# Kernel optimization log

Hardware: AMD Instinct MI355X
Metric: run time of the kernel (lower is better)

The kernel has to match this reference:

```python
import jax, jax.numpy as jnp
import numpy as np

LUT_VALS = np.array([-1.0, -0.5, -0.333333, -0.2, -0.142857, -0.090909, -0.076923,
                     0.0, 0.076923, 0.090909, 0.142857, 0.2, 0.333333, 0.5, 1.0],
                    dtype=np.float32)

B, S, IN, OUT = 4, 2048, 2048, 8192


def setup_inputs() -> dict:
    key = jax.random.key(0)
    kx, ki = jax.random.split(key)
    x = jax.random.normal(kx, (B, S, IN), dtype=jnp.float32)
    # uint8 LUT indices into the 15-entry primal grid (stored int32 for jax indexing)
    grid_indices = jax.random.randint(ki, (OUT, IN), 0, 15, dtype=jnp.int32)
    scale = jnp.float32(1.0)
    lut = jnp.asarray(LUT_VALS)
    return {"x": x, "grid_indices": grid_indices, "scale": scale, "lut": lut}


def reference(x, grid_indices, scale, lut):
    # Dequantize: gather LUT values by index, then scalar scale (GhostQuantFunction.forward)
    weights = lut[grid_indices] * scale          # [OUT, IN] fp32
    # F.linear(x, weights): y = x @ W^T
    return jnp.einsum('bsi,oi->bso', x, weights)
```

## Files before the change

kernel.cpp:

```cpp
#include <hip/hip_runtime.h>
#include <cstdint>

typedef short bf16x8 __attribute__((ext_vector_type(8)));
typedef unsigned short u16x8 __attribute__((ext_vector_type(8)));
typedef float f32x4 __attribute__((ext_vector_type(4)));
typedef __attribute__((address_space(3))) uint32_t lds_u32;
typedef const __attribute__((address_space(1))) uint32_t gbl_u32;

__device__ __forceinline__ unsigned short f2bf(float f) {
  union { float f; uint32_t u; } c; c.f = f;
  uint32_t u = c.u;
  return (unsigned short)((u + 0x7fffu + ((u >> 16) & 1u)) >> 16);
}

__global__ void cvt_x_kernel(const float* __restrict__ x,
                             unsigned short* __restrict__ y, long n) {
  long t = (long)blockIdx.x * blockDim.x + threadIdx.x;
  long base = t * 8;
  if (base >= n) return;
  const float4* p = (const float4*)(x + base);
  float4 f0 = p[0], f1 = p[1];
  u16x8 v;
  v[0] = f2bf(f0.x); v[1] = f2bf(f0.y); v[2] = f2bf(f0.z); v[3] = f2bf(f0.w);
  v[4] = f2bf(f1.x); v[5] = f2bf(f1.y); v[6] = f2bf(f1.z); v[7] = f2bf(f1.w);
  *(u16x8*)(y + base) = v;
}

__global__ void dequant_kernel(const int* __restrict__ idx,
                               const float* __restrict__ lut,
                               const float* __restrict__ scale,
                               unsigned short* __restrict__ w, long n) {
  __shared__ unsigned short slut[16];
  if (threadIdx.x < 15) slut[threadIdx.x] = f2bf(lut[threadIdx.x] * scale[0]);
  __syncthreads();
  long t = (long)blockIdx.x * blockDim.x + threadIdx.x;
  long base = t * 8;
  if (base >= n) return;
  const int4* p = (const int4*)(idx + base);
  int4 i0 = p[0], i1 = p[1];
  u16x8 v;
  v[0] = slut[i0.x]; v[1] = slut[i0.y]; v[2] = slut[i0.z]; v[3] = slut[i0.w];
  v[4] = slut[i1.x]; v[5] = slut[i1.y]; v[6] = slut[i1.z]; v[7] = slut[i1.w];
  *(u16x8*)(w + base) = v;
}

__global__ __launch_bounds__(256) void gemm_bt(
    const unsigned short* __restrict__ A,
    const unsigned short* __restrict__ B,
    float* __restrict__ C, int M, int N, int K) {
  __shared__ unsigned short lA[128 * 32];
  __shared__ unsigned short lB[128 * 32];

  const int t = threadIdx.x;
  const int l = t & 63;
  const int w = t >> 6;
  const int wm = w >> 1, wn = w & 1;
  const int bm = blockIdx.y, bn = blockIdx.x;

  f32x4 acc[4][4] = {};

  const unsigned short* gA = A + (size_t)(bm * 128 + (t >> 2)) * K + (t & 3) * 8;
  const unsigned short* gB = B + (size_t)(bn * 128 + (t >> 2)) * K + (t & 3) * 8;
  lds_u32* sA = (lds_u32*)(&lA[0]) + t * 4;
  lds_u32* sB = (lds_u32*)(&lB[0]) + t * 4;

  const int ar = wm * 64 + (l & 15);
  const int br = wn * 64 + (l & 15);
  const int ak = (l >> 4) * 8;

  for (int kt = 0; kt < K; kt += 32) {
    __syncthreads();
    __builtin_amdgcn_global_load_lds((gbl_u32*)(gA + kt),          sA,        16, 0, 0);
    __builtin_amdgcn_global_load_lds((gbl_u32*)(gA + 64 * K + kt), sA + 1024, 16, 0, 0);
    __builtin_amdgcn_global_load_lds((gbl_u32*)(gB + kt),          sB,        16, 0, 0);
    __builtin_amdgcn_global_load_lds((gbl_u32*)(gB + 64 * K + kt), sB + 1024, 16, 0, 0);
    __syncthreads();

    bf16x8 af[4], bfr[4];
#pragma unroll
    for (int i = 0; i < 4; ++i)
      af[i] = *(const bf16x8*)&lA[(ar + i * 16) * 32 + ak];
#pragma unroll
    for (int j = 0; j < 4; ++j)
      bfr[j] = *(const bf16x8*)&lB[(br + j * 16) * 32 + ak];
#pragma unroll
    for (int i = 0; i < 4; ++i)
#pragma unroll
      for (int j = 0; j < 4; ++j)
        acc[i][j] = __builtin_amdgcn_mfma_f32_16x16x32_bf16(af[i], bfr[j], acc[i][j], 0, 0, 0);
  }

  float* Cp = C + (size_t)(bm * 128 + wm * 64 + (l >> 4) * 4) * N
              + bn * 128 + wn * 64 + (l & 15);
#pragma unroll
  for (int i = 0; i < 4; ++i)
#pragma unroll
    for (int j = 0; j < 4; ++j)
#pragma unroll
      for (int r = 0; r < 4; ++r)
        Cp[(size_t)(i * 16 + r) * N + j * 16] = acc[i][j][r];
}

extern "C" void kernel_launch(void* const* d_in, const int* in_sizes, int n_in,
                              void* d_out, int out_size, void* d_ws, size_t ws_size,
                              hipStream_t stream) {
  const float* x     = (const float*)d_in[0];
  const int*   gi    = (const int*)d_in[1];
  const float* scale = (const float*)d_in[2];
  const float* lut   = (const float*)d_in[3];
  float* out = (float*)d_out;

  const int M = 8192, N = 8192, K = 2048;
  unsigned short* xb = (unsigned short*)d_ws;
  unsigned short* wb = xb + (size_t)M * K;

  long nx = (long)M * K;
  long nw = (long)N * K;
  cvt_x_kernel<<<dim3((unsigned)(nx / (256 * 8))), dim3(256), 0, stream>>>(x, xb, nx);
  dequant_kernel<<<dim3((unsigned)(nw / (256 * 8))), dim3(256), 0, stream>>>(gi, lut, scale, wb, nw);

  dim3 grid(N / 128, M / 128);
  gemm_bt<<<grid, dim3(256), 0, stream>>>(xb, wb, out, M, N, K);
}
```

Baseline: 665.2 us.

## Fuse prep kernels, use shuffle LUT, and swizzle GEMM block order

```diff
diff --git a/kernel.cpp b/kernel.cpp
--- a/kernel.cpp
+++ b/kernel.cpp
@@ -13,35 +13,40 @@
   return (unsigned short)((u + 0x7fffu + ((u >> 16) & 1u)) >> 16);
 }
 
-__global__ void cvt_x_kernel(const float* __restrict__ x,
-                             unsigned short* __restrict__ y, long n) {
-  long t = (long)blockIdx.x * blockDim.x + threadIdx.x;
-  long base = t * 8;
-  if (base >= n) return;
-  const float4* p = (const float4*)(x + base);
-  float4 f0 = p[0], f1 = p[1];
-  u16x8 v;
-  v[0] = f2bf(f0.x); v[1] = f2bf(f0.y); v[2] = f2bf(f0.z); v[3] = f2bf(f0.w);
-  v[4] = f2bf(f1.x); v[5] = f2bf(f1.y); v[6] = f2bf(f1.z); v[7] = f2bf(f1.w);
-  *(u16x8*)(y + base) = v;
-}
-
-__global__ void dequant_kernel(const int* __restrict__ idx,
-                               const float* __restrict__ lut,
-                               const float* __restrict__ scale,
-                               unsigned short* __restrict__ w, long n) {
-  __shared__ unsigned short slut[16];
-  if (threadIdx.x < 15) slut[threadIdx.x] = f2bf(lut[threadIdx.x] * scale[0]);
-  __syncthreads();
-  long t = (long)blockIdx.x * blockDim.x + threadIdx.x;
-  long base = t * 8;
-  if (base >= n) return;
-  const int4* p = (const int4*)(idx + base);
-  int4 i0 = p[0], i1 = p[1];
-  u16x8 v;
-  v[0] = slut[i0.x]; v[1] = slut[i0.y]; v[2] = slut[i0.z]; v[3] = slut[i0.w];
-  v[4] = slut[i1.x]; v[5] = slut[i1.y]; v[6] = slut[i1.z]; v[7] = slut[i1.w];
-  *(u16x8*)(w + base) = v;
+__global__ void prep_kernel(const float* __restrict__ x,
+                            const int* __restrict__ gidx,
+                            const float* __restrict__ lut,
+                            const float* __restrict__ scale,
+                            unsigned short* __restrict__ xb,
+                            unsigned short* __restrict__ wb,
+                            long nx) {
+  long bid = blockIdx.x;
+  long xblocks = nx / 2048;
+  if (bid < xblocks) {
+    long base = (bid * 256 + threadIdx.x) * 8;
+    const float4* p = (const float4*)(x + base);
+    float4 f0 = p[0], f1 = p[1];
+    u16x8 v;
+    v[0] = f2bf(f0.x); v[1] = f2bf(f0.y); v[2] = f2bf(f0.z); v[3] = f2bf(f0.w);
+    v[4] = f2bf(f1.x); v[5] = f2bf(f1.y); v[6] = f2bf(f1.z); v[7] = f2bf(f1.w);
+    *(u16x8*)(xb + base) = v;
+  } else {
+    int li = threadIdx.x & 15; if (li > 14) li = 14;
+    int ubf = (int)f2bf(lut[li] * scale[0]);
+    long base = ((bid - xblocks) * 256 + threadIdx.x) * 8;
+    const int4* p = (const int4*)(gidx + base);
+    int4 i0 = p[0], i1 = p[1];
+    u16x8 v;
+    v[0] = (unsigned short)__shfl(ubf, i0.x);
+    v[1] = (unsigned short)__shfl(ubf, i0.y);
+    v[2] = (unsigned short)__shfl(ubf, i0.z);
+    v[3] = (unsigned short)__shfl(ubf, i0.w);
+    v[4] = (unsigned short)__shfl(ubf, i1.x);
+    v[5] = (unsigned short)__shfl(ubf, i1.y);
+    v[6] = (unsigned short)__shfl(ubf, i1.z);
+    v[7] = (unsigned short)__shfl(ubf, i1.w);
+    *(u16x8*)(wb + base) = v;
+  }
 }
 
 __global__ __launch_bounds__(256) void gemm_bt(
@@ -55,7 +60,10 @@
   const int l = t & 63;
   const int w = t >> 6;
   const int wm = w >> 1, wn = w & 1;
-  const int bm = blockIdx.y, bn = blockIdx.x;
+
+  const int b = blockIdx.y * gridDim.x + blockIdx.x;
+  const int bn = ((b >> 9) << 3) | (b & 7);
+  const int bm = (b >> 3) & 63;
 
   f32x4 acc[4][4] = {};
 
@@ -116,8 +124,9 @@
 
   long nx = (long)M * K;
   long nw = (long)N * K;
-  cvt_x_kernel<<<dim3((unsigned)(nx / (256 * 8))), dim3(256), 0, stream>>>(x, xb, nx);
-  dequant_kernel<<<dim3((unsigned)(nw / (256 * 8))), dim3(256), 0, stream>>>(gi, lut, scale, wb, nw);
+  long xblocks = nx / 2048, wblocks = nw / 2048;
+  prep_kernel<<<dim3((unsigned)(xblocks + wblocks)), dim3(256), 0, stream>>>(
+      x, gi, lut, scale, xb, wb, nx);
 
   dim3 grid(N / 128, M / 128);
   gemm_bt<<<grid, dim3(256), 0, stream>>>(xb, wb, out, M, N, K);
```

After: 696.4 us. 4.7% more time.
